# Kernel tuning notes

Measured on AMD Instinct MI355X. Metric: run time of the kernel, lower is better.

The kernel has to match this reference:

```python
import jax, jax.numpy as jnp
import numpy as np

N_NODES = 100000
N_FEATS = 512
HIDDEN = 64
NUM_SAMPLES = 5
NUM_CLASSES = 16
BATCH = 16384


def setup_inputs() -> dict:
    key = jax.random.key(0)
    k1, k2, k3, k4, k5, k6, k7 = jax.random.split(key, 7)
    nodes = jax.random.randint(k1, (BATCH,), 0, N_NODES, dtype=jnp.int64) if jax.config.jax_enable_x64 else jax.random.randint(k1, (BATCH,), 0, N_NODES, dtype=jnp.int32)
    neigh_idx = jax.random.randint(k2, (N_NODES, NUM_SAMPLES), 0, N_NODES, dtype=jnp.int32)
    features = jax.random.normal(k3, (N_NODES, N_FEATS), dtype=jnp.float32)
    # xavier-uniform style init
    def xavier(k, shape):
        fan_in, fan_out = shape[1], shape[0]
        lim = jnp.sqrt(6.0 / (fan_in + fan_out)).astype(jnp.float32)
        return jax.random.uniform(k, shape, jnp.float32, -lim, lim)
    w1 = xavier(k4, (HIDDEN, 2 * N_FEATS))      # enc1 weight
    w2 = xavier(k5, (HIDDEN, 2 * HIDDEN))       # enc2 weight
    w_cls = xavier(k6, (NUM_CLASSES, HIDDEN))   # classifier weight
    return {"features": features, "w1": w1, "w2": w2, "w_cls": w_cls,
            "nodes": nodes, "neigh_idx": neigh_idx}


def reference(features, w1, w2, w_cls, nodes, neigh_idx):
    # Layer 1 (enc1, gcn=False): concat(self, mean(sampled neighbors)) -> W1 -> ReLU
    # Computed for all nodes (superset of what torch computes lazily; same values).
    neigh1 = features[neigh_idx].mean(axis=1)                      # [N, F]
    h1 = jax.nn.relu(jnp.concatenate([features, neigh1], axis=1) @ w1.T)  # [N, H]
    # Layer 2 (enc2) on the query batch
    self2 = h1[nodes]                                              # [B, H]
    neigh2 = h1[neigh_idx[nodes]].mean(axis=1)                     # [B, H]
    h2 = jax.nn.relu(jnp.concatenate([self2, neigh2], axis=1) @ w2.T)     # [B, H]
    # scores = (w_cls @ h2.T).T == h2 @ w_cls.T
    return h2 @ w_cls.T                                            # [B, C]
```

## Files before the change

kernel.cpp:

```cpp
#include <hip/hip_runtime.h>
#include <hip/hip_bf16.h>

#define N_NODES 100000
#define N_FEATS 512
#define HIDDEN 64
#define NUM_SAMPLES 5
#define NUM_CLASSES 16
#define BATCH 16384

typedef __attribute__((ext_vector_type(8))) short bf16x8;
typedef __attribute__((ext_vector_type(8))) unsigned short u16x8;
typedef __attribute__((ext_vector_type(4))) float f32x4;

static __device__ __forceinline__ float bf2f(unsigned short s) {
    unsigned int u = ((unsigned int)s) << 16;
    return __builtin_bit_cast(float, u);
}
static __device__ __forceinline__ short f2bf(float v) {
    __hip_bfloat16 b = __float2bfloat16(v);
    return *reinterpret_cast<short*>(&b);
}
static __device__ __forceinline__ int clampi(int v) {
    return ((unsigned)v < (unsigned)N_NODES) ? v : 0;
}

__global__ __launch_bounds__(256) void prep(const float* __restrict__ w1f,
                                            short* __restrict__ w1p,
                                            const int* __restrict__ nodes_i32,
                                            int* __restrict__ flag) {
    const int t = blockIdx.x * 256 + threadIdx.x;
    if (t < 64 * 1024) {
        const int j = t & 7;
        const int lane = (t >> 3) & 63;
        const int nb = (t >> 9) & 7;
        const int kk = t >> 12;
        const int l16 = lane & 15, quad = lane >> 4;
        const int cn = nb * 16 + l16;
        const int h = cn & 63, part = cn >> 6;
        w1p[t] = f2bf(w1f[h * 1024 + part * 512 + kk * 32 + quad * 8 + j]);
    }
    if (blockIdx.x == 0 && threadIdx.x == 0) {
        int odd_nonzero = 0;
        for (int i = 0; i < 64; i++)
            if (nodes_i32[2 * i + 1] != 0) odd_nonzero++;
        *flag = (odd_nonzero == 0) ? 1 : 0;
    }
}

__global__ __launch_bounds__(256) void pq_gemm(const float* __restrict__ feat,
                                               const short* __restrict__ w1p,
                                               short* __restrict__ PQ) {
    __shared__ short atile[4][16][256];
    const int wave = threadIdx.x >> 6;
    const int lane = threadIdx.x & 63;
    const int quad = lane >> 4;
    const int l16  = lane & 15;
    const int r0   = blockIdx.x * 64 + wave * 16;

    short* at = &atile[wave][0][0];

    f32x4 acc[8];
#pragma unroll
    for (int i = 0; i < 8; i++) acc[i] = (f32x4){0.f, 0.f, 0.f, 0.f};

    for (int kh = 0; kh < 2; kh++) {
        f32x4 buf[2][4];

#define ISSUE_GRP(g, slot)                                                        \
        {                                                                         \
            _Pragma("unroll")                                                     \
            for (int j = 0; j < 4; j++) {                                         \
                int rA = r0 + (g) * 4 + j;                                        \
                if (rA >= N_NODES) rA = N_NODES - 1;                              \
                buf[slot][j] = *reinterpret_cast<const f32x4*>(                   \
                    feat + (size_t)rA * N_FEATS + kh * 256 + lane * 4);           \
            }                                                                     \
        }

        ISSUE_GRP(0, 0)
        ISSUE_GRP(1, 1)
#pragma unroll
        for (int g = 0; g < 4; g++) {
            const int slot = g & 1;
#pragma unroll
            for (int j = 0; j < 4; j++) {
                const int r = g * 4 + j;
                f32x4 v = buf[slot][j];
                unsigned long long pk =
                      (unsigned long long)(unsigned short)f2bf(v[0])
                    | ((unsigned long long)(unsigned short)f2bf(v[1]) << 16)
                    | ((unsigned long long)(unsigned short)f2bf(v[2]) << 32)
                    | ((unsigned long long)(unsigned short)f2bf(v[3]) << 48);
                const int chunk = (lane >> 1) ^ (r & 7);
                *reinterpret_cast<unsigned long long*>(
                    at + r * 256 + chunk * 8 + (lane & 1) * 4) = pk;
            }
            if (g < 2) ISSUE_GRP(g + 2, slot)
        }
#undef ISSUE_GRP

#pragma unroll
        for (int kk = 0; kk < 8; kk++) {
            const int chunk = kk * 4 + quad;
            const int cs = chunk ^ (l16 & 7);
            bf16x8 afrag = *reinterpret_cast<const bf16x8*>(at + l16 * 256 + cs * 8);
            const short* bk = w1p + (size_t)(kh * 8 + kk) * 4096 + lane * 8;
#pragma unroll
            for (int nb = 0; nb < 8; nb++) {
                bf16x8 bfrag = *reinterpret_cast<const bf16x8*>(bk + nb * 512);
                acc[nb] = __builtin_amdgcn_mfma_f32_16x16x32_bf16(afrag, bfrag, acc[nb], 0, 0, 0);
            }
        }
    }

#pragma unroll
    for (int nb = 0; nb < 8; nb++) {
        const int cn = nb * 16 + l16;
#pragma unroll
        for (int r = 0; r < 4; r++) {
            const int row = r0 + quad * 4 + r;
            if (row < N_NODES) PQ[(size_t)row * 128 + cn] = f2bf(acc[nb][r]);
        }
    }
}

__global__ __launch_bounds__(256) void h1_combine(short* __restrict__ PQ,
                                                  const int* __restrict__ neigh_idx) {
    const int t = blockIdx.x * 256 + threadIdx.x;
    const int n = t >> 3;
    const int sub = t & 7;
    if (n >= N_NODES) return;

    u16x8 pv = *reinterpret_cast<const u16x8*>(PQ + (size_t)n * 128 + sub * 8);
    float s[8];
#pragma unroll
    for (int j = 0; j < 8; j++) s[j] = 0.f;
#pragma unroll
    for (int i = 0; i < NUM_SAMPLES; i++) {
        const int ni = clampi(neigh_idx[n * NUM_SAMPLES + i]);
        u16x8 qv = *reinterpret_cast<const u16x8*>(PQ + (size_t)ni * 128 + 64 + sub * 8);
#pragma unroll
        for (int j = 0; j < 8; j++) s[j] += bf2f(qv[j]);
    }
    u16x8 ov;
#pragma unroll
    for (int j = 0; j < 8; j++) {
        float v = bf2f(pv[j]) + 0.2f * s[j];
        v = v > 0.f ? v : 0.f;
        ov[j] = (unsigned short)f2bf(v);
    }
    *reinterpret_cast<u16x8*>(PQ + (size_t)n * 128 + sub * 8) = ov;
}

__global__ __launch_bounds__(256) void layer2_cls(const short* __restrict__ PQ,
                                                  const int* __restrict__ nodes_i32,
                                                  const int* __restrict__ neigh_idx,
                                                  const float* __restrict__ w2,
                                                  const float* __restrict__ wcls,
                                                  const int* __restrict__ flag,
                                                  float* __restrict__ out) {
    __shared__ float gbuf[16][128];
    __shared__ float h2buf[16][64];
    const int wave = threadIdx.x >> 6;
    const int lane = threadIdx.x & 63;
    const int is64 = *flag;
    const int b0 = blockIdx.x * 16;

#pragma unroll
    for (int it = 0; it < 4; it++) {
        const int item = wave * 4 + it;
        const int b = b0 + item;
        const int node = clampi(nodes_i32[is64 ? 2 * b : b]);
        float selfv = bf2f((unsigned short)PQ[(size_t)node * 128 + lane]);
        float ns = 0.f;
#pragma unroll
        for (int s = 0; s < NUM_SAMPLES; s++) {
            const int ni = clampi(neigh_idx[node * NUM_SAMPLES + s]);
            ns += bf2f((unsigned short)PQ[(size_t)ni * 128 + lane]);
        }
        gbuf[item][lane] = selfv;
        gbuf[item][64 + lane] = 0.2f * ns;
    }
    __syncthreads();

    float acc[4] = {0.f, 0.f, 0.f, 0.f};
    const f32x4* w2r = reinterpret_cast<const f32x4*>(w2 + lane * 128);
#pragma unroll 8
    for (int k = 0; k < 32; k++) {
        f32x4 w = w2r[k];
#pragma unroll
        for (int it = 0; it < 4; it++) {
            f32x4 g = *reinterpret_cast<const f32x4*>(&gbuf[wave * 4 + it][k * 4]);
            acc[it] += g[0] * w[0] + g[1] * w[1] + g[2] * w[2] + g[3] * w[3];
        }
    }
#pragma unroll
    for (int it = 0; it < 4; it++) {
        float h2 = acc[it] > 0.f ? acc[it] : 0.f;
        h2buf[wave * 4 + it][lane] = h2;
    }
    __syncthreads();

    if (lane < NUM_CLASSES) {
        const f32x4* wcr = reinterpret_cast<const f32x4*>(wcls + lane * 64);
#pragma unroll
        for (int it = 0; it < 4; it++) {
            const int item = wave * 4 + it;
            const f32x4* hr = reinterpret_cast<const f32x4*>(&h2buf[item][0]);
            float o = 0.f;
#pragma unroll
            for (int k = 0; k < 16; k++) {
                f32x4 h = hr[k], w = wcr[k];
                o += h[0] * w[0] + h[1] * w[1] + h[2] * w[2] + h[3] * w[3];
            }
            out[(size_t)(b0 + item) * NUM_CLASSES + lane] = o;
        }
    }
}

extern "C" void kernel_launch(void* const* d_in, const int* in_sizes, int n_in,
                              void* d_out, int out_size, void* d_ws, size_t ws_size,
                              hipStream_t stream) {
    const float* feat = nullptr;
    const float* w1 = nullptr;
    const float* w2 = nullptr;
    const float* wcls = nullptr;
    const int* nodes = nullptr;
    const int* neigh_idx = nullptr;
    for (int i = 0; i < n_in; i++) {
        switch (in_sizes[i]) {
            case 51200000: feat = (const float*)d_in[i]; break;
            case 65536:    w1 = (const float*)d_in[i]; break;
            case 8192:     w2 = (const float*)d_in[i]; break;
            case 1024:     wcls = (const float*)d_in[i]; break;
            case 16384:    nodes = (const int*)d_in[i]; break;
            case 500000:   neigh_idx = (const int*)d_in[i]; break;
            default: break;
        }
    }
    float* out = (float*)d_out;

    int* flag = (int*)d_ws;
    short* w1p = (short*)((char*)d_ws + 256);
    short* PQ  = (short*)((char*)d_ws + 256 + 64 * 1024 * sizeof(short));

    prep<<<256, 256, 0, stream>>>(w1, w1p, nodes, flag);
    pq_gemm<<<(N_NODES + 63) / 64, 256, 0, stream>>>(feat, w1p, PQ);
    h1_combine<<<(N_NODES * 8 + 255) / 256, 256, 0, stream>>>(PQ, neigh_idx);
    layer2_cls<<<BATCH / 16, 256, 0, stream>>>(PQ, nodes, neigh_idx, w2, wcls, flag, out);
}
```

Before: 360.6 us.

## Fuse four stages into one cooperative persistent kernel with grid syncs

Replaces the four separate kernel launches (weight prep, feature GEMM, layer-1 combine, layer-2 classifier) with a single cooperative persistent kernel. The stages are separated by grid-wide syncs, and work is distributed with grid-stride loops over tiles. The intent is to remove launch gaps and per-kernel tail effects. In exchange, the grid is capped at the occupancy-limited block count, which may reduce latency hiding in the memory-bound GEMM. Grid syncs also add their own cost, and the original multi-kernel path remains as a fallback if the cooperative launch fails.

```diff
diff --git a/kernel.cpp b/kernel.cpp
--- a/kernel.cpp
+++ b/kernel.cpp
@@ -1,5 +1,8 @@
 #include <hip/hip_runtime.h>
 #include <hip/hip_bf16.h>
+#include <hip/hip_cooperative_groups.h>
+
+namespace cg = cooperative_groups;
 
 #define N_NODES 100000
 #define N_FEATS 512
@@ -22,6 +25,196 @@
 }
 static __device__ __forceinline__ int clampi(int v) {
     return ((unsigned)v < (unsigned)N_NODES) ? v : 0;
+}
+
+__global__ __launch_bounds__(256, 4) void fused(
+    const float* __restrict__ feat, const float* __restrict__ w1f,
+    const float* __restrict__ w2, const float* __restrict__ wcls,
+    const int* __restrict__ nodes_i32, const int* __restrict__ neigh_idx,
+    short* __restrict__ w1p, short* __restrict__ PQ, float* __restrict__ out) {
+    cg::grid_group grid = cg::this_grid();
+    __shared__ __align__(16) char smem[32768];
+
+    const int wave = threadIdx.x >> 6;
+    const int lane = threadIdx.x & 63;
+    const int quad = lane >> 4;
+    const int l16  = lane & 15;
+    const int gsz  = gridDim.x * 256;
+
+    for (int t = blockIdx.x * 256 + threadIdx.x; t < 64 * 1024; t += gsz) {
+        const int j = t & 7;
+        const int pl = (t >> 3) & 63;
+        const int nb = (t >> 9) & 7;
+        const int kk = t >> 12;
+        const int pl16 = pl & 15, pquad = pl >> 4;
+        const int cn = nb * 16 + pl16;
+        const int h = cn & 63, part = cn >> 6;
+        w1p[t] = f2bf(w1f[h * 1024 + part * 512 + kk * 32 + pquad * 8 + j]);
+    }
+    __threadfence();
+    grid.sync();
+
+    {
+        short* at = reinterpret_cast<short*>(smem) + wave * 16 * 256;
+        const int nTiles = (N_NODES + 63) / 64;
+        for (int tile = blockIdx.x; tile < nTiles; tile += gridDim.x) {
+            const int r0 = tile * 64 + wave * 16;
+
+            f32x4 acc[8];
+#pragma unroll
+            for (int i = 0; i < 8; i++) acc[i] = (f32x4){0.f, 0.f, 0.f, 0.f};
+
+            for (int kh = 0; kh < 2; kh++) {
+                f32x4 buf[2][4];
+
+#define ISSUE_GRP(g, slot)                                                        \
+                {                                                                 \
+                    _Pragma("unroll")                                             \
+                    for (int j = 0; j < 4; j++) {                                 \
+                        int rA = r0 + (g) * 4 + j;                                \
+                        if (rA >= N_NODES) rA = N_NODES - 1;                      \
+                        buf[slot][j] = *reinterpret_cast<const f32x4*>(           \
+                            feat + (size_t)rA * N_FEATS + kh * 256 + lane * 4);   \
+                    }                                                             \
+                }
+
+                ISSUE_GRP(0, 0)
+                ISSUE_GRP(1, 1)
+#pragma unroll
+                for (int g = 0; g < 4; g++) {
+                    const int slot = g & 1;
+#pragma unroll
+                    for (int j = 0; j < 4; j++) {
+                        const int r = g * 4 + j;
+                        f32x4 v = buf[slot][j];
+                        unsigned long long pk =
+                              (unsigned long long)(unsigned short)f2bf(v[0])
+                            | ((unsigned long long)(unsigned short)f2bf(v[1]) << 16)
+                            | ((unsigned long long)(unsigned short)f2bf(v[2]) << 32)
+                            | ((unsigned long long)(unsigned short)f2bf(v[3]) << 48);
+                        const int chunk = (lane >> 1) ^ (r & 7);
+                        *reinterpret_cast<unsigned long long*>(
+                            at + r * 256 + chunk * 8 + (lane & 1) * 4) = pk;
+                    }
+                    if (g < 2) ISSUE_GRP(g + 2, slot)
+                }
+#undef ISSUE_GRP
+
+#pragma unroll
+                for (int kk = 0; kk < 8; kk++) {
+                    const int chunk = kk * 4 + quad;
+                    const int cs = chunk ^ (l16 & 7);
+                    bf16x8 afrag = *reinterpret_cast<const bf16x8*>(at + l16 * 256 + cs * 8);
+                    const short* bk = w1p + (size_t)(kh * 8 + kk) * 4096 + lane * 8;
+#pragma unroll
+                    for (int nb = 0; nb < 8; nb++) {
+                        bf16x8 bfrag = *reinterpret_cast<const bf16x8*>(bk + nb * 512);
+                        acc[nb] = __builtin_amdgcn_mfma_f32_16x16x32_bf16(afrag, bfrag, acc[nb], 0, 0, 0);
+                    }
+                }
+            }
+
+#pragma unroll
+            for (int nb = 0; nb < 8; nb++) {
+                const int cn = nb * 16 + l16;
+#pragma unroll
+                for (int r = 0; r < 4; r++) {
+                    const int row = r0 + quad * 4 + r;
+                    if (row < N_NODES) PQ[(size_t)row * 128 + cn] = f2bf(acc[nb][r]);
+                }
+            }
+        }
+    }
+    __threadfence();
+    grid.sync();
+
+    for (int t = blockIdx.x * 256 + threadIdx.x; t < N_NODES * 8; t += gsz) {
+        const int n = t >> 3;
+        const int sub = t & 7;
+        u16x8 pv = *reinterpret_cast<const u16x8*>(PQ + (size_t)n * 128 + sub * 8);
+        float s[8];
+#pragma unroll
+        for (int j = 0; j < 8; j++) s[j] = 0.f;
+#pragma unroll
+        for (int i = 0; i < NUM_SAMPLES; i++) {
+            const int ni = clampi(neigh_idx[n * NUM_SAMPLES + i]);
+            u16x8 qv = *reinterpret_cast<const u16x8*>(PQ + (size_t)ni * 128 + 64 + sub * 8);
+#pragma unroll
+            for (int j = 0; j < 8; j++) s[j] += bf2f(qv[j]);
+        }
+        u16x8 ov;
+#pragma unroll
+        for (int j = 0; j < 8; j++) {
+            float v = bf2f(pv[j]) + 0.2f * s[j];
+            v = v > 0.f ? v : 0.f;
+            ov[j] = (unsigned short)f2bf(v);
+        }
+        *reinterpret_cast<u16x8*>(PQ + (size_t)n * 128 + sub * 8) = ov;
+    }
+    __threadfence();
+    grid.sync();
+
+    {
+        float (*gbuf)[128] = reinterpret_cast<float (*)[128]>(smem);
+        float (*h2buf)[64] = reinterpret_cast<float (*)[64]>(smem + 16 * 128 * 4);
+        const int odd = nodes_i32[2 * lane + 1];
+        const int is64 = (__ballot(odd != 0) == 0ull) ? 1 : 0;
+
+        for (int grp = blockIdx.x; grp < BATCH / 16; grp += gridDim.x) {
+            const int b0 = grp * 16;
+#pragma unroll
+            for (int it = 0; it < 4; it++) {
+                const int item = wave * 4 + it;
+                const int b = b0 + item;
+                const int node = clampi(nodes_i32[is64 ? 2 * b : b]);
+                float selfv = bf2f((unsigned short)PQ[(size_t)node * 128 + lane]);
+                float ns = 0.f;
+#pragma unroll
+                for (int s = 0; s < NUM_SAMPLES; s++) {
+                    const int ni = clampi(neigh_idx[node * NUM_SAMPLES + s]);
+                    ns += bf2f((unsigned short)PQ[(size_t)ni * 128 + lane]);
+                }
+                gbuf[item][lane] = selfv;
+                gbuf[item][64 + lane] = 0.2f * ns;
+            }
+            __syncthreads();
+
+            float acc[4] = {0.f, 0.f, 0.f, 0.f};
+            const f32x4* w2r = reinterpret_cast<const f32x4*>(w2 + lane * 128);
+#pragma unroll 8
+            for (int k = 0; k < 32; k++) {
+                f32x4 w = w2r[k];
+#pragma unroll
+                for (int it = 0; it < 4; it++) {
+                    f32x4 g = *reinterpret_cast<const f32x4*>(&gbuf[wave * 4 + it][k * 4]);
+                    acc[it] += g[0] * w[0] + g[1] * w[1] + g[2] * w[2] + g[3] * w[3];
+                }
+            }
+#pragma unroll
+            for (int it = 0; it < 4; it++) {
+                float h2 = acc[it] > 0.f ? acc[it] : 0.f;
+                h2buf[wave * 4 + it][lane] = h2;
+            }
+            __syncthreads();
+
+            if (lane < NUM_CLASSES) {
+                const f32x4* wcr = reinterpret_cast<const f32x4*>(wcls + lane * 64);
+#pragma unroll
+                for (int it = 0; it < 4; it++) {
+                    const int item = wave * 4 + it;
+                    const f32x4* hr = reinterpret_cast<const f32x4*>(&h2buf[item][0]);
+                    float o = 0.f;
+#pragma unroll
+                    for (int k = 0; k < 16; k++) {
+                        f32x4 h = hr[k], w = wcr[k];
+                        o += h[0] * w[0] + h[1] * w[1] + h[2] * w[2] + h[3] * w[3];
+                    }
+                    out[(size_t)(b0 + item) * NUM_CLASSES + lane] = o;
+                }
+            }
+            __syncthreads();
+        }
+    }
 }
 
 __global__ __launch_bounds__(256) void prep(const float* __restrict__ w1f,
@@ -50,13 +243,12 @@
 __global__ __launch_bounds__(256) void pq_gemm(const float* __restrict__ feat,
                                                const short* __restrict__ w1p,
                                                short* __restrict__ PQ) {
-    __shared__ short atile[4][16][256];
+    __shared__ __align__(16) short atile[4][16][256];
     const int wave = threadIdx.x >> 6;
     const int lane = threadIdx.x & 63;
     const int quad = lane >> 4;
     const int l16  = lane & 15;
     const int r0   = blockIdx.x * 64 + wave * 16;
-
     short* at = &atile[wave][0][0];
 
     f32x4 acc[8];
@@ -65,7 +257,6 @@
 
     for (int kh = 0; kh < 2; kh++) {
         f32x4 buf[2][4];
-
 #define ISSUE_GRP(g, slot)                                                        \
         {                                                                         \
             _Pragma("unroll")                                                     \
@@ -76,7 +267,6 @@
                     feat + (size_t)rA * N_FEATS + kh * 256 + lane * 4);           \
             }                                                                     \
         }
-
         ISSUE_GRP(0, 0)
         ISSUE_GRP(1, 1)
 #pragma unroll
@@ -98,7 +288,6 @@
             if (g < 2) ISSUE_GRP(g + 2, slot)
         }
 #undef ISSUE_GRP
-
 #pragma unroll
         for (int kk = 0; kk < 8; kk++) {
             const int chunk = kk * 4 + quad;
@@ -112,7 +301,6 @@
             }
         }
     }
-
 #pragma unroll
     for (int nb = 0; nb < 8; nb++) {
         const int cn = nb * 16 + l16;
@@ -130,7 +318,6 @@
     const int n = t >> 3;
     const int sub = t & 7;
     if (n >= N_NODES) return;
-
     u16x8 pv = *reinterpret_cast<const u16x8*>(PQ + (size_t)n * 128 + sub * 8);
     float s[8];
 #pragma unroll
@@ -165,7 +352,6 @@
     const int lane = threadIdx.x & 63;
     const int is64 = *flag;
     const int b0 = blockIdx.x * 16;
-
 #pragma unroll
     for (int it = 0; it < 4; it++) {
         const int item = wave * 4 + it;
@@ -182,7 +368,6 @@
         gbuf[item][64 + lane] = 0.2f * ns;
     }
     __syncthreads();
-
     float acc[4] = {0.f, 0.f, 0.f, 0.f};
     const f32x4* w2r = reinterpret_cast<const f32x4*>(w2 + lane * 128);
 #pragma unroll 8
@@ -200,7 +385,6 @@
         h2buf[wave * 4 + it][lane] = h2;
     }
     __syncthreads();
-
     if (lane < NUM_CLASSES) {
         const f32x4* wcr = reinterpret_cast<const f32x4*>(wcls + lane * 64);
 #pragma unroll
@@ -244,8 +428,29 @@
     short* w1p = (short*)((char*)d_ws + 256);
     short* PQ  = (short*)((char*)d_ws + 256 + 64 * 1024 * sizeof(short));
 
-    prep<<<256, 256, 0, stream>>>(w1, w1p, nodes, flag);
-    pq_gemm<<<(N_NODES + 63) / 64, 256, 0, stream>>>(feat, w1p, PQ);
-    h1_combine<<<(N_NODES * 8 + 255) / 256, 256, 0, stream>>>(PQ, neigh_idx);
-    layer2_cls<<<BATCH / 16, 256, 0, stream>>>(PQ, nodes, neigh_idx, w2, wcls, flag, out);
-}
+    static int gridBlocks = 0;
+    if (gridBlocks == 0) {
+        int bpc = 0;
+        hipOccupancyMaxActiveBlocksPerMultiprocessor(&bpc, (const void*)fused, 256, 0);
+        if (bpc < 1) bpc = 1;
+        int dev = 0, cus = 0;
+        hipGetDevice(&dev);
+        hipDeviceGetAttribute(&cus, hipDeviceAttributeMultiprocessorCount, dev);
+        if (cus <= 0) cus = 256;
+        long total = (long)bpc * cus;
+        const long maxUseful = (N_NODES + 63) / 64;
+        gridBlocks = (int)(total > maxUseful ? maxUseful : total);
+    }
+
+    void* args[] = {(void*)&feat, (void*)&w1, (void*)&w2, (void*)&wcls,
+                    (void*)&nodes, (void*)&neigh_idx, (void*)&w1p, (void*)&PQ,
+                    (void*)&out};
+    hipError_t err = hipLaunchCooperativeKernel((const void*)fused, dim3(gridBlocks),
+                                                dim3(256), args, 0, stream);
+    if (err != hipSuccess) {
+        prep<<<256, 256, 0, stream>>>(w1, w1p, nodes, flag);
+        pq_gemm<<<(N_NODES + 63) / 64, 256, 0, stream>>>(feat, w1p, PQ);
+        h1_combine<<<(N_NODES * 8 + 255) / 256, 256, 0, stream>>>(PQ, neigh_idx);
+        layer2_cls<<<BATCH / 16, 256, 0, stream>>>(PQ, nodes, neigh_idx, w2, wcls, flag, out);
+    }
+}
```

New measurement: 877.6 us. +143.4%, slower.
